# Performance work log

Measured on AMD Instinct MI355X. Metric: run time of the kernel, lower is better.

Reference implementation:

```python
import jax, jax.numpy as jnp
import numpy as np

GRID = 64
BIG = 1.0e6  # threshold pushing masked-out pixels to huge distance


def _grid_dist(grid_h, grid_w):
    # pairwise euclidean distance between all grid points, (H, W, H, W)
    xs, ys = jnp.meshgrid(jnp.arange(grid_h), jnp.arange(grid_w), indexing='ij')
    coords = jnp.stack([xs.ravel(), ys.ravel()], axis=-1).astype(jnp.float32)  # (H*W, 2)
    d = jnp.sqrt(jnp.sum((coords[:, None, :] - coords[None, :, :]) ** 2, axis=-1))
    return d.reshape(grid_h, grid_w, grid_h, grid_w)


def setup_inputs() -> dict:
    key = jax.random.key(0)
    k1, k2 = jax.random.split(key)
    gt = jax.random.uniform(k1, (8, 64, 64), dtype=jnp.float32)
    pred = jax.random.uniform(k2, (8, 64, 64), dtype=jnp.float32)
    return {"gt": gt, "pred": pred}


def reference(gt, pred):
    # mode='l2_sq': sum over last axis (W for a (B,H,W) mask), then mean
    loss = jnp.mean(jnp.sum((gt - pred) ** 2, axis=-1))

    # affinity loss (dist_mat += 1.0 as in the original)
    dist = _grid_dist(GRID, GRID) + 1.0  # (64,64,64,64)

    gt_th = gt + (1.0 - gt) * BIG      # (B,H,W)
    pred_th = pred + (1.0 - pred) * BIG

    # dist_masked[b,h,w,i,j] = gt_th[b,h,w] * dist[h,w,i,j] * pred[b,i,j]
    dist_masked = gt_th[:, :, :, None, None] * dist[None] * pred[:, None, None, :, :]
    min_dist = jnp.mean(jnp.min(dist_masked, axis=(3, 4)))

    dist_masked_inv = pred_th[:, :, :, None, None] * dist[None] * gt[:, None, None, :, :]
    min_dist_inv = jnp.mean(jnp.min(dist_masked_inv, axis=(3, 4)))

    return (loss, min_dist, min_dist_inv)
```

## Files before the change

kernel.cpp:

```cpp
#include <hip/hip_runtime.h>

#define BIGV 1.0e6f

__device__ __forceinline__ float wave_max64(float v) {
    #pragma unroll
    for (int s = 32; s > 0; s >>= 1)
        v = fmaxf(v, __shfl_xor(v, s, 64));
    return v;
}

__global__ __launch_bounds__(256) void imageloss_main(
    const float* __restrict__ gt, const float* __restrict__ pred,
    float* __restrict__ ws)
{
    __shared__ float gt_s[4096];
    __shared__ float pr_s[4096];
    __shared__ float rmg[64];
    __shared__ float rmp[64];
    __shared__ float red1[256];
    __shared__ float red2[256];

    const int blk = blockIdx.x;
    const int b   = blk >> 6;
    const int h   = blk & 63;
    const int tid = threadIdx.x;

    const float* __restrict__ gt_b = gt   + b * 4096;
    const float* __restrict__ pr_b = pred + b * 4096;

    #pragma unroll
    for (int k = 0; k < 4; ++k) {
        int idx = tid + k * 256;
        float4 vg = ((const float4*)gt_b)[idx];
        float4 vp = ((const float4*)pr_b)[idx];
        ((float4*)gt_s)[idx] = vg;
        ((float4*)pr_s)[idx] = vp;
        float mg = fminf(fminf(vg.x, vg.y), fminf(vg.z, vg.w));
        float mp = fminf(fminf(vp.x, vp.y), fminf(vp.z, vp.w));
        #pragma unroll
        for (int s = 1; s < 16; s <<= 1) {
            mg = fminf(mg, __shfl_xor(mg, s, 64));
            mp = fminf(mp, __shfl_xor(mp, s, 64));
        }
        if ((tid & 15) == 0) {
            rmg[idx >> 4] = mg;
            rmp[idx >> 4] = mp;
        }
    }
    __syncthreads();

    const int w = tid & 63;
    const int c = tid >> 6;
    const float wf = (float)w;

    const int l     = w;
    const int kcand = c + 4 * l;
    const int offc  = (kcand & 1) ? ((kcand + 1) >> 1) : -(kcand >> 1);
    const int rowc  = h + offc;
    const bool valid = (l < 32) && (kcand <= 126) && ((unsigned)rowc < 64u);
    float LB1 = 3.4e38f, LB2 = 3.4e38f;
    if (valid) {
        const int adx = offc < 0 ? -offc : offc;
        const float dpl = (float)(adx + 1);
        LB1 = dpl * rmp[rowc];
        LB2 = dpl * rmg[rowc];
    }
    unsigned long long remaining = __ballot(valid);

    float m1 = 3.4e38f;
    float m2 = 3.4e38f;

    while (remaining) {
        const float T1 = wave_max64(m1);
        const float T2 = wave_max64(m2);
        unsigned long long need =
            remaining & __ballot((LB1 < T1) || (LB2 < T2));
        if (!need) break;
        const int lsel = (int)__builtin_ctzll(need);
        remaining &= ~(1ull << lsel);
        const int ksel = c + 4 * lsel;
        const int offs = (ksel & 1) ? ((ksel + 1) >> 1) : -(ksel >> 1);
        const int i    = h + offs;
        const float dx2 = (float)(offs * offs);

        const float4* __restrict__ pr4 = (const float4*)(pr_s + i * 64);
        const float4* __restrict__ gt4 = (const float4*)(gt_s + i * 64);
        #pragma unroll
        for (int j4 = 0; j4 < 16; ++j4) {
            float4 p4 = pr4[j4];
            float4 g4 = gt4[j4];
            #pragma unroll
            for (int t = 0; t < 4; ++t) {
                float jf = (float)(j4 * 4 + t);
                float dy = wf - jf;
                float d  = __builtin_amdgcn_sqrtf(fmaf(dy, dy, dx2));
                float p  = (&p4.x)[t];
                float g  = (&g4.x)[t];
                m1 = fminf(m1, fmaf(d, p, p));
                m2 = fminf(m2, fmaf(d, g, g));
            }
        }
    }

    red1[tid] = m1;
    red2[tid] = m2;
    __syncthreads();

    if (tid < 64) {
        float a1 = fminf(fminf(red1[w], red1[64 + w]), fminf(red1[128 + w], red1[192 + w]));
        float a2 = fminf(fminf(red2[w], red2[64 + w]), fminf(red2[128 + w], red2[192 + w]));

        const float g = gt_s[h * 64 + w];
        const float p = pr_s[h * 64 + w];
        const float gth = g + (1.0f - g) * BIGV;
        const float pth = p + (1.0f - p) * BIGV;

        float c1 = gth * a1;
        float c2 = pth * a2;
        float df = g - p;
        float sq = df * df;

        #pragma unroll
        for (int off = 32; off > 0; off >>= 1) {
            c1 += __shfl_down(c1, off, 64);
            c2 += __shfl_down(c2, off, 64);
            sq += __shfl_down(sq, off, 64);
        }
        if (w == 0) {
            atomicAdd(&ws[0], sq);
            atomicAdd(&ws[1], c1);
            atomicAdd(&ws[2], c2);
        }
    }
}

__global__ void imageloss_final(const float* __restrict__ ws, float* __restrict__ out)
{
    out[0] = ws[0] * (1.0f / 512.0f);
    out[1] = ws[1] * (1.0f / 32768.0f);
    out[2] = ws[2] * (1.0f / 32768.0f);
}

extern "C" void kernel_launch(void* const* d_in, const int* in_sizes, int n_in,
                              void* d_out, int out_size, void* d_ws, size_t ws_size,
                              hipStream_t stream)
{
    const float* gt   = (const float*)d_in[0];
    const float* pred = (const float*)d_in[1];
    float* out = (float*)d_out;
    float* ws  = (float*)d_ws;

    hipMemsetAsync(ws, 0, 3 * sizeof(float), stream);
    imageloss_main<<<512, 256, 0, stream>>>(gt, pred, ws);
    imageloss_final<<<1, 1, 0, stream>>>(ws, out);
}
```

Baseline: 43.62 us.

## Use 512-thread blocks with 8 waves and a single-pass pruning threshold

Doubles the block to 8 waves so each wave handles every eighth candidate row instead of every fourth. The adaptive per-row loop, which recomputed wave-max thresholds and a ballot before each row, becomes two unconditional row scans, one threshold computation, then a scan of the remaining rows whose lower bound still beats that threshold. The inner min chain is also rewritten as a tree of fminf. This cuts per-row reduction overhead and spreads the work over more waves, but the single threshold is looser and may scan more rows. Larger blocks can also reduce how many blocks fit per CU.

```diff
diff --git a/kernel.cpp b/kernel.cpp
--- a/kernel.cpp
+++ b/kernel.cpp
@@ -9,7 +9,7 @@
     return v;
 }
 
-__global__ __launch_bounds__(256) void imageloss_main(
+__global__ __launch_bounds__(512, 4) void imageloss_main(
     const float* __restrict__ gt, const float* __restrict__ pred,
     float* __restrict__ ws)
 {
@@ -17,8 +17,8 @@
     __shared__ float pr_s[4096];
     __shared__ float rmg[64];
     __shared__ float rmp[64];
-    __shared__ float red1[256];
-    __shared__ float red2[256];
+    __shared__ float red1[512];
+    __shared__ float red2[512];
 
     const int blk = blockIdx.x;
     const int b   = blk >> 6;
@@ -29,8 +29,8 @@
     const float* __restrict__ pr_b = pred + b * 4096;
 
     #pragma unroll
-    for (int k = 0; k < 4; ++k) {
-        int idx = tid + k * 256;
+    for (int k = 0; k < 2; ++k) {
+        int idx = tid + k * 512;
         float4 vg = ((const float4*)gt_b)[idx];
         float4 vp = ((const float4*)pr_b)[idx];
         ((float4*)gt_s)[idx] = vg;
@@ -53,11 +53,10 @@
     const int c = tid >> 6;
     const float wf = (float)w;
 
-    const int l     = w;
-    const int kcand = c + 4 * l;
+    const int kcand = c + 8 * w;
     const int offc  = (kcand & 1) ? ((kcand + 1) >> 1) : -(kcand >> 1);
     const int rowc  = h + offc;
-    const bool valid = (l < 32) && (kcand <= 126) && ((unsigned)rowc < 64u);
+    const bool valid = (w < 16) && (kcand <= 126) && ((unsigned)rowc < 64u);
     float LB1 = 3.4e38f, LB2 = 3.4e38f;
     if (valid) {
         const int adx = offc < 0 ? -offc : offc;
@@ -65,41 +64,53 @@
         LB1 = dpl * rmp[rowc];
         LB2 = dpl * rmg[rowc];
     }
-    unsigned long long remaining = __ballot(valid);
 
     float m1 = 3.4e38f;
     float m2 = 3.4e38f;
 
-    while (remaining) {
-        const float T1 = wave_max64(m1);
-        const float T2 = wave_max64(m2);
-        unsigned long long need =
-            remaining & __ballot((LB1 < T1) || (LB2 < T2));
-        if (!need) break;
-        const int lsel = (int)__builtin_ctzll(need);
-        remaining &= ~(1ull << lsel);
-        const int ksel = c + 4 * lsel;
+    auto scan_row = [&](int lsel) {
+        const int ksel = c + 8 * lsel;
         const int offs = (ksel & 1) ? ((ksel + 1) >> 1) : -(ksel >> 1);
         const int i    = h + offs;
         const float dx2 = (float)(offs * offs);
-
         const float4* __restrict__ pr4 = (const float4*)(pr_s + i * 64);
         const float4* __restrict__ gt4 = (const float4*)(gt_s + i * 64);
         #pragma unroll
         for (int j4 = 0; j4 < 16; ++j4) {
             float4 p4 = pr4[j4];
             float4 g4 = gt4[j4];
-            #pragma unroll
-            for (int t = 0; t < 4; ++t) {
-                float jf = (float)(j4 * 4 + t);
-                float dy = wf - jf;
-                float d  = __builtin_amdgcn_sqrtf(fmaf(dy, dy, dx2));
-                float p  = (&p4.x)[t];
-                float g  = (&g4.x)[t];
-                m1 = fminf(m1, fmaf(d, p, p));
-                m2 = fminf(m2, fmaf(d, g, g));
-            }
+            float dy0 = wf - (float)(j4 * 4 + 0);
+            float dy1 = wf - (float)(j4 * 4 + 1);
+            float dy2 = wf - (float)(j4 * 4 + 2);
+            float dy3 = wf - (float)(j4 * 4 + 3);
+            float d0 = __builtin_amdgcn_sqrtf(fmaf(dy0, dy0, dx2));
+            float d1 = __builtin_amdgcn_sqrtf(fmaf(dy1, dy1, dx2));
+            float d2 = __builtin_amdgcn_sqrtf(fmaf(dy2, dy2, dx2));
+            float d3 = __builtin_amdgcn_sqrtf(fmaf(dy3, dy3, dx2));
+            m1 = fminf(fminf(fmaf(d0, p4.x, p4.x), fmaf(d1, p4.y, p4.y)),
+                 fminf(fmaf(d2, p4.z, p4.z), fminf(fmaf(d3, p4.w, p4.w), m1)));
+            m2 = fminf(fminf(fmaf(d0, g4.x, g4.x), fmaf(d1, g4.y, g4.y)),
+                 fminf(fmaf(d2, g4.z, g4.z), fminf(fmaf(d3, g4.w, g4.w), m2)));
         }
+    };
+
+    unsigned long long remaining = __ballot(valid);
+
+    #pragma unroll 1
+    for (int p = 0; p < 2; ++p) {
+        if (!remaining) break;
+        int lsel = (int)__builtin_ctzll(remaining);
+        remaining &= remaining - 1;
+        scan_row(lsel);
+    }
+
+    const float T1 = wave_max64(m1);
+    const float T2 = wave_max64(m2);
+    unsigned long long need = remaining & __ballot((LB1 < T1) || (LB2 < T2));
+    while (need) {
+        int lsel = (int)__builtin_ctzll(need);
+        need &= need - 1;
+        scan_row(lsel);
     }
 
     red1[tid] = m1;
@@ -107,8 +118,13 @@
     __syncthreads();
 
     if (tid < 64) {
-        float a1 = fminf(fminf(red1[w], red1[64 + w]), fminf(red1[128 + w], red1[192 + w]));
-        float a2 = fminf(fminf(red2[w], red2[64 + w]), fminf(red2[128 + w], red2[192 + w]));
+        float a1 = red1[w];
+        float a2 = red2[w];
+        #pragma unroll
+        for (int q = 1; q < 8; ++q) {
+            a1 = fminf(a1, red1[q * 64 + w]);
+            a2 = fminf(a2, red2[q * 64 + w]);
+        }
 
         const float g = gt_s[h * 64 + w];
         const float p = pr_s[h * 64 + w];
@@ -151,6 +167,6 @@
     float* ws  = (float*)d_ws;
 
     hipMemsetAsync(ws, 0, 3 * sizeof(float), stream);
-    imageloss_main<<<512, 256, 0, stream>>>(gt, pred, ws);
+    imageloss_main<<<512, 512, 0, stream>>>(gt, pred, ws);
     imageloss_final<<<1, 1, 0, stream>>>(ws, out);
 }
```

Result: no change. 43.87 us (+0.6%).
